# Optimization experiments

Hardware: AMD Instinct MI355X
Metric: run time of the kernel (lower is better)

The kernel has to match this reference:

```python
import jax, jax.numpy as jnp
import numpy as np

B, N, C, K, OUT = 8, 16384, 64, 16, 64
BN_EPS = 1e-5


def setup_inputs() -> dict:
    key = jax.random.key(0)
    k1, k2, k3 = jax.random.split(key, 3)
    x = jax.random.normal(k1, (B, N, C), dtype=jnp.float32)
    idx = jax.random.randint(k2, (B, N, K), 0, N, dtype=jnp.int64)
    # fc weight, stored as (in, out) so y = agg @ W (torch Linear is x @ W.T)
    W = jax.random.normal(k3, (C, OUT), dtype=jnp.float32) * (1.0 / np.sqrt(C))
    gamma = jnp.ones((OUT,), dtype=jnp.float32)
    beta = jnp.zeros((OUT,), dtype=jnp.float32)
    return {"x": x, "idx": idx, "W": W, "gamma": gamma, "beta": beta}


def reference(x, idx, W, gamma, beta):
    Bq, Nq, Cq = x.shape
    Kq = idx.shape[-1]
    # gather neighbor features: (B, N*K, C)
    nbr = jnp.take_along_axis(x, idx.reshape(Bq, Nq * Kq, 1), axis=1)
    nbr = nbr.reshape(Bq, Nq, Kq, Cq)
    # max over neighbors, then relu
    agg = jax.nn.relu(jnp.max(nbr, axis=2))  # (B, N, C)
    # linear (no bias)
    y = agg.reshape(Bq * Nq, Cq) @ W  # (B*N, OUT)
    # BatchNorm1d in training mode: batch stats over rows, biased variance
    mean = jnp.mean(y, axis=0)
    var = jnp.mean((y - mean) ** 2, axis=0)
    y = (y - mean) * jax.lax.rsqrt(var + BN_EPS) * gamma + beta
    return y.reshape(Bq, Nq, -1)
```

## Files before the change

### kernel.cpp

```cpp
#include <hip/hip_runtime.h>

namespace {
constexpr int NPTS = 16384;
constexpr int CH   = 64;
constexpr int KNN  = 16;
constexpr int ROWS = 8 * NPTS;
constexpr float EPS = 1e-5f;
constexpr int NBLK = 2048;
constexpr int RBLK = 16;
}

typedef __attribute__((ext_vector_type(8))) short  short8;
typedef __attribute__((ext_vector_type(4))) float  f32x4;
typedef __attribute__((ext_vector_type(4))) unsigned uint4v;
typedef __attribute__((ext_vector_type(2))) unsigned uint2v;
typedef __attribute__((ext_vector_type(4))) int    int4v;

static __device__ __forceinline__ unsigned pk_bf16(float lo, float hi) {
    unsigned r;
    asm("v_cvt_pk_bf16_f32 %0, %1, %2" : "=v"(r) : "v"(lo), "v"(hi));
    return r;
}

#define PKM(D, A, B) asm volatile("v_pk_max_i16 %0, %1, %2" : "=v"(D) : "v"(A), "v"(B))

static __device__ __host__ __forceinline__ unsigned f2bf(float f) {
    unsigned u = __builtin_bit_cast(unsigned, f);
    return (u + 0x7fffu + ((u >> 16) & 1u)) >> 16;
}

static __device__ __forceinline__ void prep_wfrags(const float* __restrict__ W,
                                                   unsigned* __restrict__ wsb, int l)
{
    const int nq = l >> 4, nr = l & 15;
#pragma unroll
    for (int ct = 0; ct < 4; ++ct)
#pragma unroll
        for (int kh = 0; kh < 2; ++kh) {
            uint4v d;
#pragma unroll
            for (int dj = 0; dj < 4; ++dj) {
                const int k0 = kh * 32 + nq * 8 + dj * 2;
                unsigned lo = f2bf(W[(size_t)k0 * CH + ct * 16 + nr]);
                unsigned hi = f2bf(W[(size_t)(k0 + 1) * CH + ct * 16 + nr]);
                d[dj] = lo | (hi << 16);
            }
            ((uint4v*)wsb)[(ct * 2 + kh) * 64 + l] = d;
        }
}

__global__ __launch_bounds__(256)
void k_cvt(const float* __restrict__ x, unsigned* __restrict__ xb16,
           const float* __restrict__ W, unsigned* __restrict__ wsb)
{
    if (blockIdx.x == 0 && threadIdx.x < 64) prep_wfrags(W, wsb, threadIdx.x);
    const int batch = blockIdx.x & 7;
    const int chunk = blockIdx.x >> 3;
    const int lane8 = threadIdx.x & 7;
    const int rr    = threadIdx.x >> 3;
    const float*  xb = x    + (size_t)batch * NPTS * CH;
    unsigned*     ob = xb16 + (size_t)batch * NPTS * 32;
#pragma unroll
    for (int h = 0; h < 2; ++h) {
        const int row = chunk * 64 + h * 32 + rr;
        const f32x4* src = (const f32x4*)(xb + (size_t)row * CH + lane8 * 8);
        f32x4 v0 = src[0], v1 = src[1];
        uint4v d;
        d[0] = pk_bf16(v0[0], v0[1]);
        d[1] = pk_bf16(v0[2], v0[3]);
        d[2] = pk_bf16(v1[0], v1[1]);
        d[3] = pk_bf16(v1[2], v1[3]);
        *(uint4v*)(ob + (size_t)row * 32 + lane8 * 4) = d;
    }
}

__global__ __launch_bounds__(256)
void k_fused_bf16(const unsigned* __restrict__ xb16, const int* __restrict__ idx,
                  const unsigned* __restrict__ wsb, unsigned* __restrict__ yp,
                  float* __restrict__ partials)
{
    __shared__ __align__(16) ushort   Atile[4][16 * 64];
    __shared__ __align__(16) int      Ibuf[4][256];
    __shared__ __align__(16) unsigned Blds[2048];
    __shared__ float bs1[64], bs2[64];

    const int lane  = threadIdx.x & 63;
    const int wave  = threadIdx.x >> 6;
    const int batch = blockIdx.x & 7;
    const int chunk = blockIdx.x >> 3;

    ((uint4v*)Blds)[threadIdx.x]       = ((const uint4v*)wsb)[threadIdx.x];
    ((uint4v*)Blds)[threadIdx.x + 256] = ((const uint4v*)wsb)[threadIdx.x + 256];
    if (threadIdx.x < 64)       bs1[threadIdx.x] = 0.f;
    else if (threadIdx.x < 128) bs2[threadIdx.x - 64] = 0.f;
    __syncthreads();

    const unsigned* __restrict__ xb = xb16 + (size_t)batch * NPTS * 32;
    const int*      __restrict__ ib = idx  + (size_t)batch * NPTS * KNN;
    unsigned*       __restrict__ yb = yp   + (size_t)batch * NPTS * 32;

    const int r0 = chunk * 64 + wave * 16;
    const int g8 = lane >> 3, c8 = lane & 7;
    const int c4 = lane & 15, qq = lane >> 4;
    const unsigned off16 = (unsigned)c8 * 16u;

    int4v iq = ((const int4v*)(ib + (size_t)r0 * KNN))[lane];
    *(int4v*)&Ibuf[wave][lane * 4] = iq;

    const int4v* Ip = (const int4v*)&Ibuf[wave][0];
    int ia[16], ibx[16];
    *(int4v*)&ia[0]  = Ip[g8 * 4 + 0];       *(int4v*)&ia[4]  = Ip[g8 * 4 + 1];
    *(int4v*)&ia[8]  = Ip[g8 * 4 + 2];       *(int4v*)&ia[12] = Ip[g8 * 4 + 3];
    *(int4v*)&ibx[0] = Ip[(g8 + 8) * 4 + 0]; *(int4v*)&ibx[4] = Ip[(g8 + 8) * 4 + 1];
    *(int4v*)&ibx[8] = Ip[(g8 + 8) * 4 + 2]; *(int4v*)&ibx[12]= Ip[(g8 + 8) * 4 + 3];

    uint4v va[16], vb[16];
#pragma unroll
    for (int j = 0; j < 16; ++j)
        asm volatile("global_load_dwordx4 %0, %1, %2"
                     : "=v"(va[j])
                     : "v"((unsigned)ia[j] * 128u + off16), "s"(xb));
#pragma unroll
    for (int j = 0; j < 16; ++j)
        asm volatile("global_load_dwordx4 %0, %1, %2"
                     : "=v"(vb[j])
                     : "v"((unsigned)ibx[j] * 128u + off16), "s"(xb));

    uint4v accA = {0, 0, 0, 0}, accB = {0, 0, 0, 0};

    asm volatile("s_waitcnt vmcnt(16)" ::: "memory");
    __builtin_amdgcn_sched_barrier(0);
#pragma unroll
    for (int j = 0; j < 16; ++j) {
        PKM(accA[0], accA[0], va[j][0]); PKM(accA[1], accA[1], va[j][1]);
        PKM(accA[2], accA[2], va[j][2]); PKM(accA[3], accA[3], va[j][3]);
    }
    asm volatile("s_waitcnt vmcnt(0)" ::: "memory");
    __builtin_amdgcn_sched_barrier(0);
#pragma unroll
    for (int j = 0; j < 16; ++j) {
        PKM(accB[0], accB[0], vb[j][0]); PKM(accB[1], accB[1], vb[j][1]);
        PKM(accB[2], accB[2], vb[j][2]); PKM(accB[3], accB[3], vb[j][3]);
    }

    char* aw = (char*)&Atile[wave][0];
    *(uint4v*)(aw + ((g8 * 128 + c8 * 16) ^ (g8 << 4)))       = accA;
    *(uint4v*)(aw + (((g8 + 8) * 128 + c8 * 16) ^ (g8 << 4))) = accB;

    const int key = (c4 & 7) << 4;
    short8 a0 = *(const short8*)(aw + ((c4 * 128 + qq * 16) ^ key));
    short8 a1 = *(const short8*)(aw + ((c4 * 128 + 64 + qq * 16) ^ key));

    short8 bfr[8];
#pragma unroll
    for (int f = 0; f < 8; ++f)
        bfr[f] = __builtin_bit_cast(short8, ((const uint4v*)Blds)[f * 64 + lane]);

    f32x4 acc0 = {0,0,0,0}, acc1 = {0,0,0,0}, acc2 = {0,0,0,0}, acc3 = {0,0,0,0};
    acc0 = __builtin_amdgcn_mfma_f32_16x16x32_bf16(a0, bfr[0], acc0, 0, 0, 0);
    acc0 = __builtin_amdgcn_mfma_f32_16x16x32_bf16(a1, bfr[1], acc0, 0, 0, 0);
    acc1 = __builtin_amdgcn_mfma_f32_16x16x32_bf16(a0, bfr[2], acc1, 0, 0, 0);
    acc1 = __builtin_amdgcn_mfma_f32_16x16x32_bf16(a1, bfr[3], acc1, 0, 0, 0);
    acc2 = __builtin_amdgcn_mfma_f32_16x16x32_bf16(a0, bfr[4], acc2, 0, 0, 0);
    acc2 = __builtin_amdgcn_mfma_f32_16x16x32_bf16(a1, bfr[5], acc2, 0, 0, 0);
    acc3 = __builtin_amdgcn_mfma_f32_16x16x32_bf16(a0, bfr[6], acc3, 0, 0, 0);
    acc3 = __builtin_amdgcn_mfma_f32_16x16x32_bf16(a1, bfr[7], acc3, 0, 0, 0);

    unsigned* ypr = yb + (size_t)(r0 + qq * 4) * 32 + c4 * 2;
#pragma unroll
    for (int r = 0; r < 4; ++r) {
        uint2v pr;
        pr[0] = pk_bf16(acc0[r], acc1[r]);
        pr[1] = pk_bf16(acc2[r], acc3[r]);
        *(uint2v*)(ypr + (size_t)r * 32) = pr;
    }

#define DO_CT(CT, ACC)                                                              \
    {                                                                               \
        float s1 = (ACC[0] + ACC[1]) + (ACC[2] + ACC[3]);                           \
        float s2 = (ACC[0]*ACC[0] + ACC[1]*ACC[1]) + (ACC[2]*ACC[2] + ACC[3]*ACC[3]); \
        s1 += __shfl_xor(s1, 16); s1 += __shfl_xor(s1, 32);                         \
        s2 += __shfl_xor(s2, 16); s2 += __shfl_xor(s2, 32);                         \
        if (lane < 16) {                                                            \
            atomicAdd(&bs1[CT * 16 + lane], s1);                                    \
            atomicAdd(&bs2[CT * 16 + lane], s2);                                    \
        }                                                                           \
    }
    DO_CT(0, acc0) DO_CT(1, acc1) DO_CT(2, acc2) DO_CT(3, acc3)
#undef DO_CT

    __syncthreads();
    if (threadIdx.x < 128)
        partials[(size_t)blockIdx.x * 128 + threadIdx.x] =
            (threadIdx.x < 64) ? bs1[threadIdx.x] : bs2[threadIdx.x - 64];
}

__global__ __launch_bounds__(256)
void k_reduce(const float* __restrict__ partials, float* __restrict__ partial2)
{
    const int t = threadIdx.x;
    const int c = t & 127, h = t >> 7;
    const float* p = partials + ((size_t)blockIdx.x * 128 + h * 64) * 128 + c;
    float s = 0.f;
#pragma unroll 8
    for (int r = 0; r < 64; ++r) s += p[(size_t)r * 128];
    __shared__ float red[256];
    red[t] = s;
    __syncthreads();
    if (t < 128) partial2[(size_t)blockIdx.x * 128 + t] = red[t] + red[t + 128];
}

__global__ __launch_bounds__(256)
void k_norm_bf16(const unsigned* __restrict__ yp, float* __restrict__ y,
                 const float* __restrict__ partial2,
                 const float* __restrict__ gamma, const float* __restrict__ beta)
{
    __shared__ float s[CH], b[CH];
    if (threadIdx.x < CH) {
        const int l = threadIdx.x;
        float s1 = 0.f, s2 = 0.f;
#pragma unroll
        for (int k = 0; k < RBLK; ++k) {
            s1 += partial2[k * 128 + l];
            s2 += partial2[k * 128 + 64 + l];
        }
        const float inv_n = 1.0f / (float)ROWS;
        float mean = s1 * inv_n;
        float var  = s2 * inv_n - mean * mean;
        float sc   = gamma[l] * rsqrtf(var + EPS);
        s[l] = sc;
        b[l] = beta[l] - mean * sc;
    }
    __syncthreads();

    const size_t ntot = (size_t)ROWS * 16;
    size_t i = (size_t)blockIdx.x * blockDim.x + threadIdx.x;
    const size_t stride = (size_t)gridDim.x * blockDim.x;
    for (; i < ntot; i += stride) {
        const size_t row = i >> 4;
        const int c4 = (int)i & 15;
        uint2v p = *(const uint2v*)(yp + row * 32 + c4 * 2);
        float v0 = __uint_as_float(p[0] << 16);
        float v1 = __uint_as_float(p[0] & 0xffff0000u);
        float v2 = __uint_as_float(p[1] << 16);
        float v3 = __uint_as_float(p[1] & 0xffff0000u);
        float* yr = y + row * CH;
        yr[c4]      = fmaf(v0, s[c4],      b[c4]);
        yr[c4 + 16] = fmaf(v1, s[c4 + 16], b[c4 + 16]);
        yr[c4 + 32] = fmaf(v2, s[c4 + 32], b[c4 + 32]);
        yr[c4 + 48] = fmaf(v3, s[c4 + 48], b[c4 + 48]);
    }
}

__global__ __launch_bounds__(64)
void k_prep_fb(const float* __restrict__ W, unsigned* __restrict__ wsb,
               float* __restrict__ stats)
{
    if (threadIdx.x < 64) {
        stats[threadIdx.x] = 0.f;
        stats[64 + threadIdx.x] = 0.f;
        prep_wfrags(W, wsb, threadIdx.x);
    }
}

__global__ __launch_bounds__(256)
void k_fused_f32(const float* __restrict__ x, const int* __restrict__ idx,
                 const unsigned* __restrict__ wsb, float* __restrict__ y,
                 float* __restrict__ stats)
{
    __shared__ __align__(16) ushort Atile[4][16 * 64];
    __shared__ __align__(16) int    Ibuf[4][256];
    __shared__ float bs1[64], bs2[64];

    const int lane  = threadIdx.x & 63;
    const int wave  = threadIdx.x >> 6;
    const int batch = blockIdx.x & 7;
    const int chunk = blockIdx.x >> 3;

    if (threadIdx.x < 64)       bs1[threadIdx.x] = 0.f;
    else if (threadIdx.x < 128) bs2[threadIdx.x - 64] = 0.f;
    __syncthreads();

    const int r0 = chunk * 64 + wave * 16;
    const float* __restrict__ xb = x   + (size_t)batch * NPTS * CH;
    const int*   __restrict__ ib = idx + (size_t)batch * NPTS * KNN;
    float*       __restrict__ yb = y   + (size_t)batch * NPTS * CH;

    const int c4 = lane & 15;
    const int qq = lane >> 4;

    int4v iq = ((const int4v*)(ib + (size_t)r0 * KNN))[lane];
    *(int4v*)&Ibuf[wave][lane * 4] = iq;

    short8 bfr[8];
#pragma unroll
    for (int f = 0; f < 8; ++f)
        bfr[f] = __builtin_bit_cast(short8, ((const uint4v*)wsb)[f * 64 + lane]);

    char* aw = (char*)&Atile[wave][0];
    const f32x4* xb4 = (const f32x4*)xb;

#pragma unroll
    for (int g = 0; g < 4; ++g) {
        const int row = 4 * g + qq;
        const int* ip = &Ibuf[wave][row * KNN];
        f32x4 acc = {0.f, 0.f, 0.f, 0.f};
#pragma unroll
        for (int j = 0; j < KNN; ++j) {
            const int n = ip[j];
            f32x4 v = xb4[n * 16 + c4];
            acc[0] = fmaxf(acc[0], v[0]);
            acc[1] = fmaxf(acc[1], v[1]);
            acc[2] = fmaxf(acc[2], v[2]);
            acc[3] = fmaxf(acc[3], v[3]);
        }
        uint2v pw;
        pw[0] = pk_bf16(acc[0], acc[1]);
        pw[1] = pk_bf16(acc[2], acc[3]);
        const int wb = ((row * 128) + c4 * 8) ^ ((row & 7) << 4);
        *(uint2v*)(aw + wb) = pw;
    }

    const int key = (c4 & 7) << 4;
    short8 a0 = *(const short8*)(aw + ((c4 * 128 + qq * 16) ^ key));
    short8 a1 = *(const short8*)(aw + ((c4 * 128 + 64 + qq * 16) ^ key));

    f32x4 acc0 = {0,0,0,0}, acc1 = {0,0,0,0}, acc2 = {0,0,0,0}, acc3 = {0,0,0,0};
    acc0 = __builtin_amdgcn_mfma_f32_16x16x32_bf16(a0, bfr[0], acc0, 0, 0, 0);
    acc0 = __builtin_amdgcn_mfma_f32_16x16x32_bf16(a1, bfr[1], acc0, 0, 0, 0);
    acc1 = __builtin_amdgcn_mfma_f32_16x16x32_bf16(a0, bfr[2], acc1, 0, 0, 0);
    acc1 = __builtin_amdgcn_mfma_f32_16x16x32_bf16(a1, bfr[3], acc1, 0, 0, 0);
    acc2 = __builtin_amdgcn_mfma_f32_16x16x32_bf16(a0, bfr[4], acc2, 0, 0, 0);
    acc2 = __builtin_amdgcn_mfma_f32_16x16x32_bf16(a1, bfr[5], acc2, 0, 0, 0);
    acc3 = __builtin_amdgcn_mfma_f32_16x16x32_bf16(a0, bfr[6], acc3, 0, 0, 0);
    acc3 = __builtin_amdgcn_mfma_f32_16x16x32_bf16(a1, bfr[7], acc3, 0, 0, 0);

    float* yrow = yb + (size_t)(r0 + qq * 4) * CH + c4;
#define DO_CT(CT, ACC)                                                              \
    {                                                                               \
        yrow[0 * CH + CT * 16] = ACC[0];                                            \
        yrow[1 * CH + CT * 16] = ACC[1];                                            \
        yrow[2 * CH + CT * 16] = ACC[2];                                            \
        yrow[3 * CH + CT * 16] = ACC[3];                                            \
        float s1 = (ACC[0] + ACC[1]) + (ACC[2] + ACC[3]);                           \
        float s2 = (ACC[0]*ACC[0] + ACC[1]*ACC[1]) + (ACC[2]*ACC[2] + ACC[3]*ACC[3]); \
        s1 += __shfl_xor(s1, 16); s1 += __shfl_xor(s1, 32);                         \
        s2 += __shfl_xor(s2, 16); s2 += __shfl_xor(s2, 32);                         \
        if (lane < 16) {                                                            \
            atomicAdd(&bs1[CT * 16 + lane], s1);                                    \
            atomicAdd(&bs2[CT * 16 + lane], s2);                                    \
        }                                                                           \
    }
    DO_CT(0, acc0) DO_CT(1, acc1) DO_CT(2, acc2) DO_CT(3, acc3)
#undef DO_CT

    __syncthreads();
    if (threadIdx.x < 64)        atomicAdd(&stats[threadIdx.x], bs1[threadIdx.x]);
    else if (threadIdx.x < 128)  atomicAdd(&stats[threadIdx.x], bs2[threadIdx.x - 64]);
}

__global__ __launch_bounds__(256)
void k_norm_f32(float* __restrict__ y, const float* __restrict__ stats,
                const float* __restrict__ gamma, const float* __restrict__ beta)
{
    __shared__ float s[CH], b[CH];
    if (threadIdx.x < CH) {
        const int l = threadIdx.x;
        const float inv_n = 1.0f / (float)ROWS;
        float mean = stats[l] * inv_n;
        float var  = stats[64 + l] * inv_n - mean * mean;
        float sc   = gamma[l] * rsqrtf(var + EPS);
        s[l] = sc;
        b[l] = beta[l] - mean * sc;
    }
    __syncthreads();

    f32x4* p = (f32x4*)y;
    const size_t ntot = (size_t)ROWS * CH / 4;
    size_t i = (size_t)blockIdx.x * blockDim.x + threadIdx.x;
    const size_t stride = (size_t)gridDim.x * blockDim.x;
    for (; i < ntot; i += stride) {
        f32x4 v = p[i];
        const int c0 = ((int)i & 15) * 4;
        v[0] = fmaf(v[0], s[c0],     b[c0]);
        v[1] = fmaf(v[1], s[c0 + 1], b[c0 + 1]);
        v[2] = fmaf(v[2], s[c0 + 2], b[c0 + 2]);
        v[3] = fmaf(v[3], s[c0 + 3], b[c0 + 3]);
        p[i] = v;
    }
}

extern "C" void kernel_launch(void* const* d_in, const int* in_sizes, int n_in,
                              void* d_out, int out_size, void* d_ws, size_t ws_size,
                              hipStream_t stream)
{
    const float* x     = (const float*)d_in[0];
    const int*   idx   = (const int*)d_in[1];
    const float* W     = (const float*)d_in[2];
    const float* gamma = (const float*)d_in[3];
    const float* beta  = (const float*)d_in[4];

    float*    y     = (float*)d_out;
    float*    stats = (float*)d_ws;
    unsigned* wsb   = (unsigned*)(stats + 256);
    char*     base  = (char*)d_ws + 16384;
    unsigned* xb16  = (unsigned*)base;
    float*    parts = (float*)(base + (size_t)ROWS * CH * 2);
    float*    part2 = parts + (size_t)NBLK * 128;
    unsigned* yp    = (unsigned*)(part2 + (size_t)RBLK * 128);

    const size_t need = 16384 + (size_t)ROWS * CH * 2
                      + (size_t)NBLK * 128 * 4 + (size_t)RBLK * 128 * 4
                      + (size_t)ROWS * CH * 2;

    if (ws_size >= need) {
        k_cvt<<<dim3(2048), dim3(256), 0, stream>>>(x, xb16, W, wsb);
        k_fused_bf16<<<dim3(NBLK), dim3(256), 0, stream>>>(xb16, idx, wsb, yp, parts);
        k_reduce<<<dim3(RBLK), dim3(256), 0, stream>>>(parts, part2);
        k_norm_bf16<<<dim3(2048), dim3(256), 0, stream>>>(yp, y, part2, gamma, beta);
    } else {
        k_prep_fb<<<dim3(1), dim3(64), 0, stream>>>(W, wsb, stats);
        k_fused_f32<<<dim3(2048), dim3(256), 0, stream>>>(x, idx, wsb, y, stats);
        k_norm_f32<<<dim3(2048), dim3(256), 0, stream>>>(y, stats, gamma, beta);
    }
}
```

Measured before the change: 44.26 us.

## Process two row tiles per block and prefetch the second tile's gathers

Each block now covers 128 rows instead of 64, so the grid shrinks to 1024 blocks. The second tile's neighbor indices and gather loads are issued before the first tile's max, MFMA, store and stats work, so that work hides some of the gather latency. BN statistics are kept in registers across both tiles and flushed to LDS atomics once. The weight fragment load and the per-block partials write are now amortized over twice as many rows, and the reduce kernel is adjusted to the smaller partials count. In exchange, register pressure rises and there are fewer blocks to spread latency across.

```diff
diff --git a/kernel.cpp b/kernel.cpp
--- a/kernel.cpp
+++ b/kernel.cpp
@@ -6,7 +6,7 @@
 constexpr int KNN  = 16;
 constexpr int ROWS = 8 * NPTS;
 constexpr float EPS = 1e-5f;
-constexpr int NBLK = 2048;
+constexpr int NBLK = 1024;
 constexpr int RBLK = 16;
 }
 
@@ -99,14 +99,23 @@
     const int*      __restrict__ ib = idx  + (size_t)batch * NPTS * KNN;
     unsigned*       __restrict__ yb = yp   + (size_t)batch * NPTS * 32;
 
-    const int r0 = chunk * 64 + wave * 16;
+    const int r0 = chunk * 128 + wave * 16;
     const int g8 = lane >> 3, c8 = lane & 7;
     const int c4 = lane & 15, qq = lane >> 4;
     const unsigned off16 = (unsigned)c8 * 16u;
-
-    int4v iq = ((const int4v*)(ib + (size_t)r0 * KNN))[lane];
-    *(int4v*)&Ibuf[wave][lane * 4] = iq;
-
+    const int key = (c4 & 7) << 4;
+    char* aw = (char*)&Atile[wave][0];
+
+    short8 bfr[8];
+#pragma unroll
+    for (int f = 0; f < 8; ++f)
+        bfr[f] = __builtin_bit_cast(short8, ((const uint4v*)Blds)[f * 64 + lane]);
+
+    float sC1[4] = {0.f, 0.f, 0.f, 0.f};
+    float sC2[4] = {0.f, 0.f, 0.f, 0.f};
+
+    int4v iq0 = ((const int4v*)(ib + (size_t)r0 * KNN))[lane];
+    *(int4v*)&Ibuf[wave][lane * 4] = iq0;
     const int4v* Ip = (const int4v*)&Ibuf[wave][0];
     int ia[16], ibx[16];
     *(int4v*)&ia[0]  = Ip[g8 * 4 + 0];       *(int4v*)&ia[4]  = Ip[g8 * 4 + 1];
@@ -118,77 +127,110 @@
 #pragma unroll
     for (int j = 0; j < 16; ++j)
         asm volatile("global_load_dwordx4 %0, %1, %2"
-                     : "=v"(va[j])
-                     : "v"((unsigned)ia[j] * 128u + off16), "s"(xb));
+                     : "=v"(va[j]) : "v"((unsigned)ia[j] * 128u + off16), "s"(xb));
 #pragma unroll
     for (int j = 0; j < 16; ++j)
         asm volatile("global_load_dwordx4 %0, %1, %2"
-                     : "=v"(vb[j])
-                     : "v"((unsigned)ibx[j] * 128u + off16), "s"(xb));
+                     : "=v"(vb[j]) : "v"((unsigned)ibx[j] * 128u + off16), "s"(xb));
+
+    int4v iq1 = ((const int4v*)(ib + (size_t)(r0 + 64) * KNN))[lane];
+
+    asm volatile("s_waitcnt vmcnt(0)" ::: "memory");
+    __builtin_amdgcn_sched_barrier(0);
 
     uint4v accA = {0, 0, 0, 0}, accB = {0, 0, 0, 0};
-
-    asm volatile("s_waitcnt vmcnt(16)" ::: "memory");
-    __builtin_amdgcn_sched_barrier(0);
 #pragma unroll
     for (int j = 0; j < 16; ++j) {
         PKM(accA[0], accA[0], va[j][0]); PKM(accA[1], accA[1], va[j][1]);
         PKM(accA[2], accA[2], va[j][2]); PKM(accA[3], accA[3], va[j][3]);
     }
-    asm volatile("s_waitcnt vmcnt(0)" ::: "memory");
-    __builtin_amdgcn_sched_barrier(0);
 #pragma unroll
     for (int j = 0; j < 16; ++j) {
         PKM(accB[0], accB[0], vb[j][0]); PKM(accB[1], accB[1], vb[j][1]);
         PKM(accB[2], accB[2], vb[j][2]); PKM(accB[3], accB[3], vb[j][3]);
     }
 
-    char* aw = (char*)&Atile[wave][0];
-    *(uint4v*)(aw + ((g8 * 128 + c8 * 16) ^ (g8 << 4)))       = accA;
-    *(uint4v*)(aw + (((g8 + 8) * 128 + c8 * 16) ^ (g8 << 4))) = accB;
-
-    const int key = (c4 & 7) << 4;
-    short8 a0 = *(const short8*)(aw + ((c4 * 128 + qq * 16) ^ key));
-    short8 a1 = *(const short8*)(aw + ((c4 * 128 + 64 + qq * 16) ^ key));
-
-    short8 bfr[8];
-#pragma unroll
-    for (int f = 0; f < 8; ++f)
-        bfr[f] = __builtin_bit_cast(short8, ((const uint4v*)Blds)[f * 64 + lane]);
-
-    f32x4 acc0 = {0,0,0,0}, acc1 = {0,0,0,0}, acc2 = {0,0,0,0}, acc3 = {0,0,0,0};
-    acc0 = __builtin_amdgcn_mfma_f32_16x16x32_bf16(a0, bfr[0], acc0, 0, 0, 0);
-    acc0 = __builtin_amdgcn_mfma_f32_16x16x32_bf16(a1, bfr[1], acc0, 0, 0, 0);
-    acc1 = __builtin_amdgcn_mfma_f32_16x16x32_bf16(a0, bfr[2], acc1, 0, 0, 0);
-    acc1 = __builtin_amdgcn_mfma_f32_16x16x32_bf16(a1, bfr[3], acc1, 0, 0, 0);
-    acc2 = __builtin_amdgcn_mfma_f32_16x16x32_bf16(a0, bfr[4], acc2, 0, 0, 0);
-    acc2 = __builtin_amdgcn_mfma_f32_16x16x32_bf16(a1, bfr[5], acc2, 0, 0, 0);
-    acc3 = __builtin_amdgcn_mfma_f32_16x16x32_bf16(a0, bfr[6], acc3, 0, 0, 0);
-    acc3 = __builtin_amdgcn_mfma_f32_16x16x32_bf16(a1, bfr[7], acc3, 0, 0, 0);
-
-    unsigned* ypr = yb + (size_t)(r0 + qq * 4) * 32 + c4 * 2;
-#pragma unroll
-    for (int r = 0; r < 4; ++r) {
-        uint2v pr;
-        pr[0] = pk_bf16(acc0[r], acc1[r]);
-        pr[1] = pk_bf16(acc2[r], acc3[r]);
-        *(uint2v*)(ypr + (size_t)r * 32) = pr;
-    }
-
-#define DO_CT(CT, ACC)                                                              \
+    *(int4v*)&Ibuf[wave][lane * 4] = iq1;
+    *(int4v*)&ia[0]  = Ip[g8 * 4 + 0];       *(int4v*)&ia[4]  = Ip[g8 * 4 + 1];
+    *(int4v*)&ia[8]  = Ip[g8 * 4 + 2];       *(int4v*)&ia[12] = Ip[g8 * 4 + 3];
+    *(int4v*)&ibx[0] = Ip[(g8 + 8) * 4 + 0]; *(int4v*)&ibx[4] = Ip[(g8 + 8) * 4 + 1];
+    *(int4v*)&ibx[8] = Ip[(g8 + 8) * 4 + 2]; *(int4v*)&ibx[12]= Ip[(g8 + 8) * 4 + 3];
+
+#pragma unroll
+    for (int j = 0; j < 16; ++j)
+        asm volatile("global_load_dwordx4 %0, %1, %2"
+                     : "=v"(va[j]) : "v"((unsigned)ia[j] * 128u + off16), "s"(xb));
+#pragma unroll
+    for (int j = 0; j < 16; ++j)
+        asm volatile("global_load_dwordx4 %0, %1, %2"
+                     : "=v"(vb[j]) : "v"((unsigned)ibx[j] * 128u + off16), "s"(xb));
+    __builtin_amdgcn_sched_barrier(0);
+
+#define TILE_TAIL(RBASE)                                                            \
     {                                                                               \
-        float s1 = (ACC[0] + ACC[1]) + (ACC[2] + ACC[3]);                           \
-        float s2 = (ACC[0]*ACC[0] + ACC[1]*ACC[1]) + (ACC[2]*ACC[2] + ACC[3]*ACC[3]); \
-        s1 += __shfl_xor(s1, 16); s1 += __shfl_xor(s1, 32);                         \
-        s2 += __shfl_xor(s2, 16); s2 += __shfl_xor(s2, 32);                         \
-        if (lane < 16) {                                                            \
-            atomicAdd(&bs1[CT * 16 + lane], s1);                                    \
-            atomicAdd(&bs2[CT * 16 + lane], s2);                                    \
-        }                                                                           \
-    }
-    DO_CT(0, acc0) DO_CT(1, acc1) DO_CT(2, acc2) DO_CT(3, acc3)
-#undef DO_CT
-
+        *(uint4v*)(aw + ((g8 * 128 + c8 * 16) ^ (g8 << 4)))       = accA;           \
+        *(uint4v*)(aw + (((g8 + 8) * 128 + c8 * 16) ^ (g8 << 4))) = accB;           \
+        short8 a0 = *(const short8*)(aw + ((c4 * 128 + qq * 16) ^ key));            \
+        short8 a1 = *(const short8*)(aw + ((c4 * 128 + 64 + qq * 16) ^ key));       \
+        f32x4 acc0 = {0,0,0,0}, acc1 = {0,0,0,0}, acc2 = {0,0,0,0}, acc3 = {0,0,0,0}; \
+        acc0 = __builtin_amdgcn_mfma_f32_16x16x32_bf16(a0, bfr[0], acc0, 0, 0, 0);  \
+        acc0 = __builtin_amdgcn_mfma_f32_16x16x32_bf16(a1, bfr[1], acc0, 0, 0, 0);  \
+        acc1 = __builtin_amdgcn_mfma_f32_16x16x32_bf16(a0, bfr[2], acc1, 0, 0, 0);  \
+        acc1 = __builtin_amdgcn_mfma_f32_16x16x32_bf16(a1, bfr[3], acc1, 0, 0, 0);  \
+        acc2 = __builtin_amdgcn_mfma_f32_16x16x32_bf16(a0, bfr[4], acc2, 0, 0, 0);  \
+        acc2 = __builtin_amdgcn_mfma_f32_16x16x32_bf16(a1, bfr[5], acc2, 0, 0, 0);  \
+        acc3 = __builtin_amdgcn_mfma_f32_16x16x32_bf16(a0, bfr[6], acc3, 0, 0, 0);  \
+        acc3 = __builtin_amdgcn_mfma_f32_16x16x32_bf16(a1, bfr[7], acc3, 0, 0, 0);  \
+        unsigned* ypr = yb + (size_t)((RBASE) + qq * 4) * 32 + c4 * 2;              \
+        { uint2v pr; pr[0] = pk_bf16(acc0[0], acc1[0]);                             \
+          pr[1] = pk_bf16(acc2[0], acc3[0]); *(uint2v*)(ypr + 0)  = pr; }           \
+        { uint2v pr; pr[0] = pk_bf16(acc0[1], acc1[1]);                             \
+          pr[1] = pk_bf16(acc2[1], acc3[1]); *(uint2v*)(ypr + 32) = pr; }           \
+        { uint2v pr; pr[0] = pk_bf16(acc0[2], acc1[2]);                             \
+          pr[1] = pk_bf16(acc2[2], acc3[2]); *(uint2v*)(ypr + 64) = pr; }           \
+        { uint2v pr; pr[0] = pk_bf16(acc0[3], acc1[3]);                             \
+          pr[1] = pk_bf16(acc2[3], acc3[3]); *(uint2v*)(ypr + 96) = pr; }           \
+        sC1[0] += (acc0[0] + acc0[1]) + (acc0[2] + acc0[3]);                        \
+        sC2[0] += (acc0[0]*acc0[0] + acc0[1]*acc0[1]) + (acc0[2]*acc0[2] + acc0[3]*acc0[3]); \
+        sC1[1] += (acc1[0] + acc1[1]) + (acc1[2] + acc1[3]);                        \
+        sC2[1] += (acc1[0]*acc1[0] + acc1[1]*acc1[1]) + (acc1[2]*acc1[2] + acc1[3]*acc1[3]); \
+        sC1[2] += (acc2[0] + acc2[1]) + (acc2[2] + acc2[3]);                        \
+        sC2[2] += (acc2[0]*acc2[0] + acc2[1]*acc2[1]) + (acc2[2]*acc2[2] + acc2[3]*acc2[3]); \
+        sC1[3] += (acc3[0] + acc3[1]) + (acc3[2] + acc3[3]);                        \
+        sC2[3] += (acc3[0]*acc3[0] + acc3[1]*acc3[1]) + (acc3[2]*acc3[2] + acc3[3]*acc3[3]); \
+    }
+
+    TILE_TAIL(r0)
+
+    asm volatile("s_waitcnt vmcnt(4)" ::: "memory");
+    __builtin_amdgcn_sched_barrier(0);
+
+    accA[0] = accA[1] = accA[2] = accA[3] = 0u;
+    accB[0] = accB[1] = accB[2] = accB[3] = 0u;
+#pragma unroll
+    for (int j = 0; j < 16; ++j) {
+        PKM(accA[0], accA[0], va[j][0]); PKM(accA[1], accA[1], va[j][1]);
+        PKM(accA[2], accA[2], va[j][2]); PKM(accA[3], accA[3], va[j][3]);
+    }
+#pragma unroll
+    for (int j = 0; j < 16; ++j) {
+        PKM(accB[0], accB[0], vb[j][0]); PKM(accB[1], accB[1], vb[j][1]);
+        PKM(accB[2], accB[2], vb[j][2]); PKM(accB[3], accB[3], vb[j][3]);
+    }
+
+    TILE_TAIL(r0 + 64)
+#undef TILE_TAIL
+
+#pragma unroll
+    for (int ct = 0; ct < 4; ++ct) {
+        float s1 = sC1[ct], s2 = sC2[ct];
+        s1 += __shfl_xor(s1, 16); s1 += __shfl_xor(s1, 32);
+        s2 += __shfl_xor(s2, 16); s2 += __shfl_xor(s2, 32);
+        if (lane < 16) {
+            atomicAdd(&bs1[ct * 16 + lane], s1);
+            atomicAdd(&bs2[ct * 16 + lane], s2);
+        }
+    }
     __syncthreads();
     if (threadIdx.x < 128)
         partials[(size_t)blockIdx.x * 128 + threadIdx.x] =
@@ -200,10 +242,10 @@
 {
     const int t = threadIdx.x;
     const int c = t & 127, h = t >> 7;
-    const float* p = partials + ((size_t)blockIdx.x * 128 + h * 64) * 128 + c;
+    const float* p = partials + ((size_t)blockIdx.x * 64 + h * 32) * 128 + c;
     float s = 0.f;
 #pragma unroll 8
-    for (int r = 0; r < 64; ++r) s += p[(size_t)r * 128];
+    for (int r = 0; r < 32; ++r) s += p[(size_t)r * 128];
     __shared__ float red[256];
     red[t] = s;
     __syncthreads();
```

Result: faster. 42.87 us (-3.1%).
